# Performance work log

Measured on AMD Instinct MI355X. Metric: run time of the kernel, lower is better.

The kernel has to match this reference:

```python
import jax, jax.numpy as jnp
import numpy as np

N_NODES = 50000
N_EDGES = 800000
D = 64
D_OUT = 64


def setup_inputs() -> dict:
    key = jax.random.key(0)
    ks = jax.random.split(key, 7)
    h_src = jax.random.normal(ks[0], (N_NODES, D), dtype=jnp.float32)
    h_dst = jax.random.normal(ks[1], (N_NODES, D), dtype=jnp.float32)
    e = jax.random.normal(ks[2], (N_EDGES, D), dtype=jnp.float32)
    src = jax.random.randint(ks[3], (N_EDGES,), 0, N_NODES, dtype=jnp.int32)
    dst = jax.random.randint(ks[4], (N_EDGES,), 0, N_NODES, dtype=jnp.int32)
    W = jax.random.normal(ks[5], (D_OUT, 2 * D), dtype=jnp.float32) * 0.05  # nn.Linear weight [out, in]
    b = jax.random.normal(ks[6], (D_OUT,), dtype=jnp.float32) * 0.05
    return {"h_src": h_src, "h_dst": h_dst, "e": e, "src": src, "dst": dst, "W": W, "b": b}


def reference(h_src, h_dst, e, src, dst, W, b):
    # u_dot_e: per-edge dot product between gathered src features and edge features
    h_u = h_src[src]                                   # [E, D] gather
    score = jnp.sum(h_u * e, axis=-1)                  # [E]
    exp_s = jnp.exp(score)                             # raw exp, as in original (no max-subtract)
    # segment-sum exp over dst nodes, then edge-wise normalize (edge softmax)
    denom = jax.ops.segment_sum(exp_s, dst, num_segments=N_NODES)  # [N]
    pi = exp_s / denom[dst]                            # [E]
    # weighted neighbor aggregation: sum_e pi * h_src[src] into dst
    msg = h_u * pi[:, None]                            # [E, D]
    h_sum = jax.ops.segment_sum(msg, dst, num_segments=N_NODES)    # [N, D]
    # concat self features with aggregated neighbors, then linear
    h_total = jnp.concatenate([h_dst, h_sum], axis=1)  # [N, 2D]
    return h_total @ W.T + b                           # [N, D_OUT]
```

## Files before the change

kernel.cpp:

```cpp
#include <hip/hip_runtime.h>

#define N_NODES 50000
#define N_EDGES 800000
#define D 64
#define CAP 64

typedef float vf4 __attribute__((ext_vector_type(4)));

__global__ __launch_bounds__(256) void k1_score_bucket(
    const vf4* __restrict__ h_src4, const vf4* __restrict__ e4,
    const int* __restrict__ src, const int* __restrict__ dst,
    int* __restrict__ count, int2* __restrict__ slots) {
    int t = threadIdx.x;
    int i = blockIdx.x * 16 + (t >> 4);
    int l16 = t & 15;
    int s = src[i];
    int d = dst[i];
    vf4 u  = h_src4[(size_t)s * 16 + l16];
    vf4 ev = __builtin_nontemporal_load(&e4[(size_t)i * 16 + l16]);
    float p = u[0]*ev[0] + u[1]*ev[1] + u[2]*ev[2] + u[3]*ev[3];
    p += __shfl_xor(p, 1, 16);
    p += __shfl_xor(p, 2, 16);
    p += __shfl_xor(p, 4, 16);
    p += __shfl_xor(p, 8, 16);
    if (l16 == 0) {
        float w = __expf(p);
        int pos = atomicAdd(&count[d], 1);
        if (pos < CAP)
            slots[(size_t)d * CAP + pos] = make_int2(s, __float_as_int(w));
    }
}

__global__ __launch_bounds__(256) void k23_agg_linear(
    const vf4* __restrict__ h_src4, const vf4* __restrict__ h_dst4,
    const int* __restrict__ count, const int2* __restrict__ slots,
    const float* __restrict__ W, const float* __restrict__ b,
    float* __restrict__ out) {
    __shared__ float Wl[128 * 65];
    __shared__ __align__(16) float ht[16][132];
    int t = threadIdx.x;
    for (int i = t; i < 128 * 64; i += 256) {
        int o = i >> 7, k = i & 127;
        Wl[k * 65 + o] = W[i];
    }
    int node0 = blockIdx.x * 16;
    int n = t >> 4;
    int l16 = t & 15;
    int node = node0 + n;
    *(vf4*)&ht[n][l16 * 4] = h_dst4[(size_t)node * 16 + l16];

    int cnt = count[node];
    cnt = cnt < CAP ? cnt : CAP;
    const int2* row = slots + (size_t)node * CAP;
    vf4 acc = {0.f, 0.f, 0.f, 0.f};
    float dsum = 0.f;
    int2 se = make_int2(0, 0);
    if (l16 < cnt) se = row[l16];
    for (int base = 0; base < cnt; base += 16) {
        int2 cur = se;
        int nxt = base + 16;
        se = make_int2(0, 0);
        if (nxt + l16 < cnt) se = row[nxt + l16];
        vf4 us[16];
        #pragma unroll
        for (int j = 0; j < 16; ++j) {
            int sj = __shfl(cur.x, j, 16);
            us[j] = h_src4[(size_t)sj * 16 + l16];
        }
        #pragma unroll
        for (int j = 0; j < 16; ++j) {
            float wj = __int_as_float(__shfl(cur.y, j, 16));
            acc += wj * us[j];
            dsum += wj;
        }
    }
    float inv = (cnt > 0) ? 1.f / dsum : 0.f;
    acc *= inv;
    *(vf4*)&ht[n][64 + l16 * 4] = acc;
    __syncthreads();

    int o = t & 63;
    int g = t >> 6;
    float bias = b[o];
    float a0 = bias, a1 = bias, a2 = bias, a3 = bias;
    const float* h0 = &ht[g * 4 + 0][0];
    const float* h1 = &ht[g * 4 + 1][0];
    const float* h2 = &ht[g * 4 + 2][0];
    const float* h3 = &ht[g * 4 + 3][0];
    #pragma unroll
    for (int k = 0; k < 128; k += 4) {
        float w0 = Wl[(k + 0) * 65 + o];
        float w1 = Wl[(k + 1) * 65 + o];
        float w2 = Wl[(k + 2) * 65 + o];
        float w3 = Wl[(k + 3) * 65 + o];
        vf4 p0 = *(const vf4*)&h0[k];
        vf4 p1 = *(const vf4*)&h1[k];
        vf4 p2 = *(const vf4*)&h2[k];
        vf4 p3 = *(const vf4*)&h3[k];
        a0 += p0[0]*w0 + p0[1]*w1 + p0[2]*w2 + p0[3]*w3;
        a1 += p1[0]*w0 + p1[1]*w1 + p1[2]*w2 + p1[3]*w3;
        a2 += p2[0]*w0 + p2[1]*w1 + p2[2]*w2 + p2[3]*w3;
        a3 += p3[0]*w0 + p3[1]*w1 + p3[2]*w2 + p3[3]*w3;
    }
    __builtin_nontemporal_store(a0, &out[(size_t)(node0 + g * 4 + 0) * 64 + o]);
    __builtin_nontemporal_store(a1, &out[(size_t)(node0 + g * 4 + 1) * 64 + o]);
    __builtin_nontemporal_store(a2, &out[(size_t)(node0 + g * 4 + 2) * 64 + o]);
    __builtin_nontemporal_store(a3, &out[(size_t)(node0 + g * 4 + 3) * 64 + o]);
}

extern "C" void kernel_launch(void* const* d_in, const int* in_sizes, int n_in,
                              void* d_out, int out_size, void* d_ws, size_t ws_size,
                              hipStream_t stream) {
    const float* h_src = (const float*)d_in[0];
    const float* h_dst = (const float*)d_in[1];
    const float* e     = (const float*)d_in[2];
    const int*   src   = (const int*)d_in[3];
    const int*   dst   = (const int*)d_in[4];
    const float* W     = (const float*)d_in[5];
    const float* b     = (const float*)d_in[6];
    float* out = (float*)d_out;

    auto align256 = [](size_t x) { return (x + 255) & ~(size_t)255; };
    char* ws = (char*)d_ws;
    int*  count = (int*)ws;
    int2* slots = (int2*)(ws + align256((size_t)N_NODES * 4));

    hipMemsetAsync(count, 0, (size_t)N_NODES * 4, stream);

    k1_score_bucket<<<N_EDGES / 16, 256, 0, stream>>>(
        (const vf4*)h_src, (const vf4*)e, src, dst, count, slots);
    k23_agg_linear<<<N_NODES / 16, 256, 0, stream>>>(
        (const vf4*)h_src, (const vf4*)h_dst, count, slots, W, b, out);
}
```

Before: 381.7 us.

## Process 16 edges per lane group in score kernel with batched loads and parallel atomics

The score/bucket kernel now gives each 16-lane group 16 edges instead of one. Each lane loads its own edge's src/dst and issues its atomicAdd up front, so the atomics run in parallel across lanes instead of serialised on lane 0. The h_src and e rows are then loaded in batches of 8 to raise memory-level parallelism, and the grid shrinks by 16x. The cost is more registers per thread, which the added occupancy hint in launch bounds constrains, and fewer blocks in flight.

```diff
diff --git a/kernel.cpp b/kernel.cpp
--- a/kernel.cpp
+++ b/kernel.cpp
@@ -7,28 +7,44 @@
 
 typedef float vf4 __attribute__((ext_vector_type(4)));
 
-__global__ __launch_bounds__(256) void k1_score_bucket(
+__global__ __launch_bounds__(256, 4) void k1_score_bucket(
     const vf4* __restrict__ h_src4, const vf4* __restrict__ e4,
     const int* __restrict__ src, const int* __restrict__ dst,
     int* __restrict__ count, int2* __restrict__ slots) {
     int t = threadIdx.x;
-    int i = blockIdx.x * 16 + (t >> 4);
-    int l16 = t & 15;
-    int s = src[i];
-    int d = dst[i];
-    vf4 u  = h_src4[(size_t)s * 16 + l16];
-    vf4 ev = __builtin_nontemporal_load(&e4[(size_t)i * 16 + l16]);
-    float p = u[0]*ev[0] + u[1]*ev[1] + u[2]*ev[2] + u[3]*ev[3];
-    p += __shfl_xor(p, 1, 16);
-    p += __shfl_xor(p, 2, 16);
-    p += __shfl_xor(p, 4, 16);
-    p += __shfl_xor(p, 8, 16);
-    if (l16 == 0) {
-        float w = __expf(p);
-        int pos = atomicAdd(&count[d], 1);
-        if (pos < CAP)
-            slots[(size_t)d * CAP + pos] = make_int2(s, __float_as_int(w));
+    int g = t >> 4, l16 = t & 15;
+    int ebase = blockIdx.x * 256 + g * 16;
+    int myedge = ebase + l16;
+    int s = src[myedge];
+    int d = dst[myedge];
+    int pos = atomicAdd(&count[d], 1);
+    float myw = 0.f;
+    #pragma unroll
+    for (int b = 0; b < 16; b += 8) {
+        vf4 us[8], evs[8];
+        #pragma unroll
+        for (int j = 0; j < 8; ++j) {
+            int jj = b + j;
+            int sj = __shfl(s, jj, 16);
+            us[j]  = h_src4[(size_t)sj * 16 + l16];
+            evs[j] = __builtin_nontemporal_load(
+                &e4[(size_t)(ebase + jj) * 16 + l16]);
+        }
+        #pragma unroll
+        for (int j = 0; j < 8; ++j) {
+            int jj = b + j;
+            vf4 u = us[j], ev = evs[j];
+            float p = u[0]*ev[0] + u[1]*ev[1] + u[2]*ev[2] + u[3]*ev[3];
+            p += __shfl_xor(p, 1, 16);
+            p += __shfl_xor(p, 2, 16);
+            p += __shfl_xor(p, 4, 16);
+            p += __shfl_xor(p, 8, 16);
+            float w = __expf(p);
+            myw = (jj == l16) ? w : myw;
+        }
     }
+    if (pos < CAP)
+        slots[(size_t)d * CAP + pos] = make_int2(s, __float_as_int(myw));
 }
 
 __global__ __launch_bounds__(256) void k23_agg_linear(
@@ -127,7 +143,7 @@
 
     hipMemsetAsync(count, 0, (size_t)N_NODES * 4, stream);
 
-    k1_score_bucket<<<N_EDGES / 16, 256, 0, stream>>>(
+    k1_score_bucket<<<N_EDGES / 256, 256, 0, stream>>>(
         (const vf4*)h_src, (const vf4*)e, src, dst, count, slots);
     k23_agg_linear<<<N_NODES / 16, 256, 0, stream>>>(
         (const vf4*)h_src, (const vf4*)h_dst, count, slots, W, b, out);
```

Result: no change. 387.0 us (+1.4%).
